# Performance work log

Measured on AMD Instinct MI355X. Metric: run time of the kernel, lower is better.

The kernel has to match this reference:

```python
import jax, jax.numpy as jnp
import numpy as np

SCALE, R_MAX, ALPHA = 16, 8, 2.0
HL, WL, C_FEAT = 16, 16, 384
HH, WH = HL * SCALE, WL * SCALE


def bilinear_resize(img, out_h, out_w):
    """PyTorch F.interpolate(mode='bilinear', align_corners=False, antialias=False).
    img: [..., H, W] -> [..., out_h, out_w]."""
    H, W = img.shape[-2], img.shape[-1]
    ys = jnp.maximum((jnp.arange(out_h, dtype=jnp.float32) + 0.5) * (H / out_h) - 0.5, 0.0)
    xs = jnp.maximum((jnp.arange(out_w, dtype=jnp.float32) + 0.5) * (W / out_w) - 0.5, 0.0)
    y0 = jnp.floor(ys).astype(jnp.int32)
    x0 = jnp.floor(xs).astype(jnp.int32)
    y1 = jnp.minimum(y0 + 1, H - 1)
    x1 = jnp.minimum(x0 + 1, W - 1)
    wy = (ys - y0)[:, None]
    wx = (xs - x0)[None, :]
    g = lambda yi, xi: img[..., yi[:, None], xi[None, :]]
    return ((1 - wy) * (1 - wx) * g(y0, x0) + (1 - wy) * wx * g(y0, x1)
            + wy * (1 - wx) * g(y1, x0) + wy * wx * g(y1, x1))


def jbu_forward(feat_lr, guide_hr, sx_raw, sy_raw, th_raw, sr_raw):
    C, Hl, Wl = feat_lr.shape[1], feat_lr.shape[2], feat_lr.shape[3]
    Hh, Wh = guide_hr.shape[2], guide_hr.shape[3]
    scale, R_max, alpha = SCALE, R_MAX, ALPHA
    NEG = -1e30  # finite stand-in for -inf (keeps grads NaN-free)

    # parameter transforms from the module
    sx = jnp.exp(sx_raw[0, 0])
    sy = jnp.exp(sy_raw[0, 0])
    th = jnp.pi * jnp.tanh(th_raw[0, 0])
    sr = jnp.exp(sr_raw[0, 0])

    Y, X = jnp.meshgrid(jnp.arange(Hh, dtype=jnp.float32),
                        jnp.arange(Wh, dtype=jnp.float32), indexing='ij')
    u = (Y + 0.5) / scale - 0.5
    v = (X + 0.5) / scale - 0.5
    uc = jnp.clip(jnp.round(u), 0, Hl - 1).astype(jnp.int32)
    vc = jnp.clip(jnp.round(v), 0, Wl - 1).astype(jnp.int32)

    sigma_eff_hr = bilinear_resize(jnp.maximum(sx, sy), Hh, Wh)
    R_map = jnp.clip(jnp.ceil(alpha * sigma_eff_hr), 1.0, float(R_max))  # [Hh,Wh]

    offs = jnp.arange(-R_max, R_max + 1, dtype=jnp.int32)
    dYg, dXg = jnp.meshgrid(offs, offs, indexing='ij')
    dY = dYg.reshape(-1)[:, None, None]  # [N,1,1]
    dX = dXg.reshape(-1)[:, None, None]

    Ui = jnp.clip(uc[None] + dY, 0, Hl - 1)  # [N,Hh,Wh]
    Vi = jnp.clip(vc[None] + dX, 0, Wl - 1)
    idx = Ui * Wl + Vi                       # flat LR index per (neighbor, HR pixel)
    gat = lambda mp: mp.reshape(-1)[idx]

    sxg = jnp.maximum(gat(sx), 1e-6)
    syg = jnp.maximum(gat(sy), 1e-6)
    thg = gat(th)
    srg = jnp.maximum(gat(sr), 1e-6)

    dx = X[None] - ((Vi.astype(jnp.float32) + 0.5) * scale - 0.5)
    dyv = Y[None] - ((Ui.astype(jnp.float32) + 0.5) * scale - 0.5)
    ct, st = jnp.cos(thg), jnp.sin(thg)
    a = dx * ct + dyv * st
    b = -dx * st + dyv * ct

    guide_lr = bilinear_resize(guide_hr[0], Hl, Wl)  # [3,Hl,Wl]
    g_diff2 = sum((guide_hr[0, c][None] - gat(guide_lr[c])) ** 2 for c in range(3))

    log_w = (-a * a / (2 * sxg ** 2 + 1e-8)
             - b * b / (2 * syg ** 2 + 1e-8)
             - g_diff2 / (2.0 * srg ** 2 + 1e-8))  # [N,Hh,Wh]

    mask = (dY * dY + dX * dX).astype(jnp.float32) <= R_map[None] ** 2
    log_w = jnp.where(mask, log_w, NEG)

    # numerically stable softmax over neighbors (== online-softmax result)
    m = log_w.max(axis=0)
    s = jnp.exp(log_w - m[None])  # masked entries underflow to 0
    den = s.sum(axis=0)           # [Hh,Wh]

    # num[c,h,w] = sum_n s[n,h,w] * feat[idx[n,h,w], c]
    # scatter neighbor weights by LR pixel, then one GEMM with the LR features
    N = idx.shape[0]
    idx2 = idx.reshape(N, Hh * Wh)
    cols = jnp.arange(Hh * Wh, dtype=jnp.int32)[None, :]
    acc = jnp.zeros((Hl * Wl, Hh * Wh), jnp.float32).at[idx2, cols].add(s.reshape(N, -1))
    feat_flat = feat_lr[0].reshape(C, Hl * Wl)  # [C, P]
    num = jnp.einsum('cp,pq->cq', feat_flat, acc).reshape(C, Hh, Wh)

    return (num / jnp.maximum(den, 1e-8)[None])[None]  # [1,C,Hh,Wh]


def setup_inputs() -> dict:
    key = jax.random.key(0)
    k1, k2, k3, k4, k5, k6 = jax.random.split(key, 6)
    feat_lr = jax.random.normal(k1, (1, C_FEAT, HL, WL), jnp.float32)
    guide_hr = jax.random.uniform(k2, (1, 3, HH, WH), dtype=jnp.float32)
    log_sigma = float(np.log(16.0))
    log_sigma_r = float(np.log(0.12))
    sx_raw = log_sigma + 0.1 * jax.random.normal(k3, (1, 1, HL, WL), jnp.float32)
    sy_raw = log_sigma + 0.1 * jax.random.normal(k4, (1, 1, HL, WL), jnp.float32)
    th_raw = 0.1 * jax.random.normal(k5, (1, 1, HL, WL), jnp.float32)
    sr_raw = log_sigma_r + 0.1 * jax.random.normal(k6, (1, 1, HL, WL), jnp.float32)
    return {"feat_lr": feat_lr, "guide_hr": guide_hr, "sx_raw": sx_raw,
            "sy_raw": sy_raw, "th_raw": th_raw, "sr_raw": sr_raw}


def reference(feat_lr, guide_hr, sx_raw, sy_raw, th_raw, sr_raw):
    return jbu_forward(feat_lr, guide_hr, sx_raw, sy_raw, th_raw, sr_raw)
```

## Files before the change

kernel.cpp:

```cpp
#include <hip/hip_runtime.h>
#include <math.h>

#define NEG_BIG  (-1e30f)
#define NEG_H16  (-60000.0f)

typedef _Float16 half8  __attribute__((ext_vector_type(8)));
typedef _Float16 half2v __attribute__((ext_vector_type(2)));
typedef float    floatx4 __attribute__((ext_vector_type(4)));

__global__ __launch_bounds__(256) void setup_all(
    const float* __restrict__ feat, const float* __restrict__ guide,
    const float* __restrict__ sx_raw, const float* __restrict__ sy_raw,
    const float* __restrict__ th_raw, const float* __restrict__ sr_raw,
    _Float16* __restrict__ feat16, float4* __restrict__ PA,
    float4* __restrict__ PB, float* __restrict__ PS,
    _Float16* __restrict__ LCtab)
{
    const int b = blockIdx.x, t = threadIdx.x;
    if (b < 384) {
        int i = b*256 + t;
        feat16[i] = (_Float16)feat[i];
        return;
    }
    if (b == 384) {
        float sx = expf(sx_raw[t]);
        float sy = expf(sy_raw[t]);
        float th = 3.14159265358979323846f * tanhf(th_raw[t]);
        float sr = expf(sr_raw[t]);
        float sxg = fmaxf(sx, 1e-6f), syg = fmaxf(sy, 1e-6f), srg = fmaxf(sr, 1e-6f);
        float iA = 1.f / (2.f*sxg*sxg + 1e-8f);
        float iB = 1.f / (2.f*syg*syg + 1e-8f);
        float iC = 1.f / (2.f*srg*srg + 1e-8f);
        float ct = cosf(th), st = sinf(th);
        float A2 = iA*ct*ct + iB*st*st;
        float B2 = 2.f*ct*st*(iA - iB);
        float C2 = iA*st*st + iB*ct*ct;
        PA[t] = make_float4(-A2, -B2, -C2, -iC);
        int i = t >> 4, j = t & 15;
        int y0 = 16*i + 7, x0 = 16*j + 7;
        float g[3];
#pragma unroll
        for (int c = 0; c < 3; ++c) {
            const float* gp = guide + c*65536;
            g[c] = 0.25f*(gp[y0*256 + x0]     + gp[y0*256 + x0 + 1] +
                          gp[(y0+1)*256 + x0] + gp[(y0+1)*256 + x0 + 1]);
        }
        PB[t] = make_float4(2.f*iC*g[0], 2.f*iC*g[1], 2.f*iC*g[2],
                            -iC*(g[0]*g[0] + g[1]*g[1] + g[2]*g[2]));
        PS[t] = fmaxf(sx, sy);
        return;
    }
    const int tb  = b - 385;
    const int uc  = tb >> 3;
    const int vc0 = (tb & 7) << 1;
    const int Pu  = t >> 4;
    const int col = t & 15;
    const int Rt  = (col >> 1) + 1;
    const int vc  = vc0 + (col & 1);
    const int R2  = Rt * Rt;
    int ylo = (Pu == 0)  ? -8 : (Pu - uc);
    int yhi = (Pu == 15) ?  8 : (Pu - uc);
    ylo = max(ylo, -8); yhi = min(yhi, 8);
    int cnt[16];
#pragma unroll
    for (int Pv = 1; Pv < 15; ++Pv) {
        int d = Pv - vc;
        int lim = R2 - d*d;
        int c = 0;
        if (lim >= 0 && ylo <= yhi) {
            int s = (int)sqrtf((float)lim);
            c = max(0, min(yhi, s) - max(ylo, -s) + 1);
        }
        cnt[Pv] = c;
    }
    cnt[0] = 0;
    if (-vc >= -8) {
        for (int dY = ylo; dY <= yhi; ++dY) {
            int lim = R2 - dY*dY;
            if (lim >= 0) {
                int r = (int)sqrtf((float)lim);
                cnt[0] += max(0, min(-vc, r) + r + 1);
            }
        }
    }
    cnt[15] = 0;
    if (15 - vc <= 8) {
        for (int dY = ylo; dY <= yhi; ++dY) {
            int lim = R2 - dY*dY;
            if (lim >= 0) {
                int r = (int)sqrtf((float)lim);
                cnt[15] += max(0, r - max(15 - vc, -r) + 1);
            }
        }
    }
    _Float16* dst = LCtab + (size_t)tb * 4096;
#pragma unroll
    for (int Pv = 0; Pv < 16; ++Pv)
        dst[(Pu*16 + Pv)*16 + col] = (_Float16)
            ((cnt[Pv] > 0) ? __logf((float)cnt[Pv]) : NEG_H16);
}

__global__ __launch_bounds__(256, 4) void jbu_main(
    const float* __restrict__ guide, const _Float16* __restrict__ feat16,
    const float4* __restrict__ PA, const float4* __restrict__ PB,
    const float* __restrict__ PS, const _Float16* __restrict__ LCtab,
    float* __restrict__ out)
{
    __shared__ float4 sPA[256];
    __shared__ float4 sPB[256];
    __shared__ __align__(16) _Float16 LCh[4096];
    __shared__ __align__(16) _Float16 Wb[32][256];
    __shared__ float redM[4][32];
    __shared__ float redD[4][32];

    const int t = threadIdx.x;
    const int q    = t & 31;
    const int grp  = t >> 5;
    const int wv   = t >> 6;
    const int Y    = blockIdx.y;
    const int X0   = blockIdx.x << 5;
    const int X    = X0 + q;
    const float Yf = (float)Y, Xf = (float)X;
    const int uc   = Y >> 4;

    sPA[t] = PA[t];
    sPB[t] = PB[t];
    {
        const float4* Lsrc =
            (const float4*)(LCtab + (size_t)(uc*8 + blockIdx.x) * 4096);
        ((float4*)LCh)[t]       = Lsrc[t];
        ((float4*)LCh)[t + 256] = Lsrc[t + 256];
    }

    float u = (Yf + 0.5f)*0.0625f - 0.5f;
    float v = (Xf + 0.5f)*0.0625f - 0.5f;
    float ysc = fmaxf(u, 0.f), xsc = fmaxf(v, 0.f);
    int y0 = (int)ysc, x0 = (int)xsc;
    int y1 = min(y0 + 1, 15), x1 = min(x0 + 1, 15);
    float wy = ysc - (float)y0, wx = xsc - (float)x0;
    float s00 = PS[y0*16 + x0], s01 = PS[y0*16 + x1];
    float s10 = PS[y1*16 + x0], s11 = PS[y1*16 + x1];
    float sig = (1.f - wy)*((1.f - wx)*s00 + wx*s01)
              +        wy *((1.f - wx)*s10 + wx*s11);
    float Rf = fminf(fmaxf(ceilf(2.f*sig), 1.f), 8.f);
    const int colq = ((int)Rf - 1)*2 + (q >> 4);

    const float g0 = guide[          (Y << 8) + X];
    const float g1 = guide[ 65536 + ((Y << 8) + X)];
    const float g2 = guide[131072 + ((Y << 8) + X)];
    const float g2s = g0*g0 + g1*g1 + g2*g2;

    __syncthreads();

    const int pbase = grp << 5;
    const float dy0  = Yf - (32.f*(float)grp + 7.5f);
    const float dy1  = dy0 - 16.f;
    const float dy20 = dy0*dy0, dy21 = dy1*dy1;
    float lw[32];
    float mloc = NEG_BIG;
#pragma unroll
    for (int col = 0; col < 16; ++col) {
        float dx    = Xf - (16.f*(float)col + 7.5f);
        float dx2   = dx*dx;
        float dxdy0 = dx*dy0, dxdy1 = dx*dy1;
#pragma unroll
        for (int row = 0; row < 2; ++row) {
            int pi = row*16 + col;
            int p  = pbase + pi;
            float4 A = sPA[p];
            float4 B = sPB[p];
            float w = fmaf(B.x, g0, B.w);
            w = fmaf(B.y, g1, w);
            w = fmaf(B.z, g2, w);
            w = fmaf(A.w, g2s, w);
            w = fmaf(A.x, dx2, w);
            w = fmaf(A.y, row ? dxdy1 : dxdy0, w);
            w = fmaf(A.z, row ? dy21  : dy20,  w);
            w += (float)LCh[p*16 + colq];
            lw[pi] = w;
            mloc = fmaxf(mloc, w);
        }
    }
    mloc = fmaxf(mloc, __shfl_xor(mloc, 32, 64));
    redM[wv][q] = mloc;
    __syncthreads();
    float m = fmaxf(fmaxf(redM[0][q], redM[1][q]),
                    fmaxf(redM[2][q], redM[3][q]));

    float dloc = 0.f;
#pragma unroll
    for (int pi = 0; pi < 32; pi += 2) {
        int p = pbase + pi;
        float e0 = __expf(lw[pi]     - m);
        float e1 = __expf(lw[pi + 1] - m);
        half2v hh; hh[0] = (_Float16)e0; hh[1] = (_Float16)e1;
        int chunk = ((p >> 3) ^ q) & 31;
        *(half2v*)&Wb[q][chunk*8 + (p & 7)] = hh;
        dloc += (float)hh[0] + (float)hh[1];
    }
    dloc += __shfl_xor(dloc, 32, 64);
    redD[wv][q] = dloc;
    __syncthreads();

    const int lane = t & 63;
    const int mrow = lane & 15;
    const int quad = lane >> 4;
    const int c0   = wv * 96;

    float idv[2];
#pragma unroll
    for (int nt = 0; nt < 2; ++nt) {
        int pix = nt*16 + mrow;
        float den = redD[0][pix] + redD[1][pix] + redD[2][pix] + redD[3][pix];
        idv[nt] = 1.f / fmaxf(den, 1e-8f);
    }

    floatx4 acc[6][2] = {};
    const _Float16* fbase = feat16 + (c0 + mrow)*256 + quad*8;

#pragma unroll
    for (int ks = 0; ks < 8; ++ks) {
        half8 a[6];
#pragma unroll
        for (int mt = 0; mt < 6; ++mt)
            a[mt] = *(const half8*)(fbase + mt*16*256 + ks*32);
        half8 b[2];
#pragma unroll
        for (int nt = 0; nt < 2; ++nt) {
            int pix = nt*16 + mrow;
            int chunk = ((ks*4 + quad) ^ pix) & 31;
            b[nt] = *(const half8*)(&Wb[pix][chunk*8]);
        }
#pragma unroll
        for (int mt = 0; mt < 6; ++mt)
#pragma unroll
            for (int nt = 0; nt < 2; ++nt)
                acc[mt][nt] = __builtin_amdgcn_mfma_f32_16x16x32_f16(
                    a[mt], b[nt], acc[mt][nt], 0, 0, 0);
    }

    float* Sf = (float*)LCh + (wv << 9);
    const int sch = lane >> 3;
    const int spg = lane & 7;
    const int outcol = (Y << 8) + X0;
#pragma unroll
    for (int mt = 0; mt < 6; ++mt) {
#pragma unroll
        for (int nt = 0; nt < 2; ++nt)
#pragma unroll
            for (int r = 0; r < 4; ++r)
                Sf[(quad*4 + r)*32 + nt*16 + mrow] = acc[mt][nt][r] * idv[nt];
#pragma unroll
        for (int j = 0; j < 2; ++j) {
            float4 vv = *(const float4*)&Sf[(j*8 + sch)*32 + spg*4];
            *(float4*)(out + (size_t)(c0 + mt*16 + j*8 + sch)*65536
                           + outcol + spg*4) = vv;
        }
    }
}

extern "C" void kernel_launch(void* const* d_in, const int* in_sizes, int n_in,
                              void* d_out, int out_size, void* d_ws, size_t ws_size,
                              hipStream_t stream)
{
    const float* feat   = (const float*)d_in[0];
    const float* guide  = (const float*)d_in[1];
    const float* sx_raw = (const float*)d_in[2];
    const float* sy_raw = (const float*)d_in[3];
    const float* th_raw = (const float*)d_in[4];
    const float* sr_raw = (const float*)d_in[5];
    float* out = (float*)d_out;

    char* ws = (char*)d_ws;
    _Float16* feat16 = (_Float16*)ws;
    float4*   PA     = (float4*)(ws + 196608);
    float4*   PB     = (float4*)(ws + 200704);
    float*    PS     = (float*)(ws + 204800);
    _Float16* LCtab  = (_Float16*)(ws + 205824);

    setup_all<<<513, 256, 0, stream>>>(feat, guide, sx_raw, sy_raw, th_raw,
                                       sr_raw, feat16, PA, PB, PS, LCtab);
    jbu_main<<<dim3(8, 256), 256, 0, stream>>>(guide, feat16, PA, PB, PS,
                                               LCtab, out);
}
```

Baseline: 158.6 us.

## Use 512-thread blocks in main kernel and vectorize feat fp16 conversion

The main kernel now runs 512 threads per block. Each thread scores 16 LR positions instead of 32, and each wave computes 48 output channels instead of 96, which halves the per-thread register arrays. The output staging buffer moves to the Wb region behind an extra barrier, and the reductions widen to 8 waves. The setup kernel converts the features to fp16 with 8-wide vector loads and stores, using far fewer blocks. The trade-off is a larger block with more barrier cost in exchange for lower register pressure per thread.

```diff
diff --git a/kernel.cpp b/kernel.cpp
--- a/kernel.cpp
+++ b/kernel.cpp
@@ -17,12 +17,17 @@
     _Float16* __restrict__ LCtab)
 {
     const int b = blockIdx.x, t = threadIdx.x;
-    if (b < 384) {
-        int i = b*256 + t;
-        feat16[i] = (_Float16)feat[i];
+    if (b < 48) {
+        int i = (b*256 + t)*8;
+        float4 f0 = *(const float4*)(feat + i);
+        float4 f1 = *(const float4*)(feat + i + 4);
+        half8 h;
+        h[0]=(_Float16)f0.x; h[1]=(_Float16)f0.y; h[2]=(_Float16)f0.z; h[3]=(_Float16)f0.w;
+        h[4]=(_Float16)f1.x; h[5]=(_Float16)f1.y; h[6]=(_Float16)f1.z; h[7]=(_Float16)f1.w;
+        *(half8*)(feat16 + i) = h;
         return;
     }
-    if (b == 384) {
+    if (b == 48) {
         float sx = expf(sx_raw[t]);
         float sy = expf(sy_raw[t]);
         float th = 3.14159265358979323846f * tanhf(th_raw[t]);
@@ -50,7 +55,7 @@
         PS[t] = fmaxf(sx, sy);
         return;
     }
-    const int tb  = b - 385;
+    const int tb  = b - 49;
     const int uc  = tb >> 3;
     const int vc0 = (tb & 7) << 1;
     const int Pu  = t >> 4;
@@ -100,36 +105,35 @@
             ((cnt[Pv] > 0) ? __logf((float)cnt[Pv]) : NEG_H16);
 }
 
-__global__ __launch_bounds__(256, 4) void jbu_main(
+__global__ __launch_bounds__(512) void jbu_main(
     const float* __restrict__ guide, const _Float16* __restrict__ feat16,
     const float4* __restrict__ PA, const float4* __restrict__ PB,
     const float* __restrict__ PS, const _Float16* __restrict__ LCtab,
     float* __restrict__ out)
 {
+    __shared__ __align__(16) _Float16 Wb[32][256];
     __shared__ float4 sPA[256];
     __shared__ float4 sPB[256];
     __shared__ __align__(16) _Float16 LCh[4096];
-    __shared__ __align__(16) _Float16 Wb[32][256];
-    __shared__ float redM[4][32];
-    __shared__ float redD[4][32];
-
-    const int t = threadIdx.x;
-    const int q    = t & 31;
-    const int grp  = t >> 5;
-    const int wv   = t >> 6;
-    const int Y    = blockIdx.y;
-    const int X0   = blockIdx.x << 5;
-    const int X    = X0 + q;
+    __shared__ float redM[8][32];
+    __shared__ float redD[8][32];
+
+    const int t   = threadIdx.x;
+    const int q   = t & 31;
+    const int grp = t >> 5;
+    const int wv  = t >> 6;
+    const int Y   = blockIdx.y;
+    const int X0  = blockIdx.x << 5;
+    const int X   = X0 + q;
     const float Yf = (float)Y, Xf = (float)X;
     const int uc   = Y >> 4;
 
-    sPA[t] = PA[t];
-    sPB[t] = PB[t];
+    if (t < 256) sPA[t] = PA[t];
+    else         sPB[t & 255] = PB[t & 255];
     {
         const float4* Lsrc =
             (const float4*)(LCtab + (size_t)(uc*8 + blockIdx.x) * 4096);
-        ((float4*)LCh)[t]       = Lsrc[t];
-        ((float4*)LCh)[t + 256] = Lsrc[t + 256];
+        ((float4*)LCh)[t] = Lsrc[t];
     }
 
     float u = (Yf + 0.5f)*0.0625f - 0.5f;
@@ -152,50 +156,45 @@
 
     __syncthreads();
 
-    const int pbase = grp << 5;
-    const float dy0  = Yf - (32.f*(float)grp + 7.5f);
-    const float dy1  = dy0 - 16.f;
-    const float dy20 = dy0*dy0, dy21 = dy1*dy1;
-    float lw[32];
+    const int pbase = grp << 4;
+    const float dy  = Yf - (16.f*(float)grp + 7.5f);
+    const float dy2 = dy*dy;
+    float lw[16];
     float mloc = NEG_BIG;
 #pragma unroll
     for (int col = 0; col < 16; ++col) {
-        float dx    = Xf - (16.f*(float)col + 7.5f);
-        float dx2   = dx*dx;
-        float dxdy0 = dx*dy0, dxdy1 = dx*dy1;
-#pragma unroll
-        for (int row = 0; row < 2; ++row) {
-            int pi = row*16 + col;
-            int p  = pbase + pi;
-            float4 A = sPA[p];
-            float4 B = sPB[p];
-            float w = fmaf(B.x, g0, B.w);
-            w = fmaf(B.y, g1, w);
-            w = fmaf(B.z, g2, w);
-            w = fmaf(A.w, g2s, w);
-            w = fmaf(A.x, dx2, w);
-            w = fmaf(A.y, row ? dxdy1 : dxdy0, w);
-            w = fmaf(A.z, row ? dy21  : dy20,  w);
-            w += (float)LCh[p*16 + colq];
-            lw[pi] = w;
-            mloc = fmaxf(mloc, w);
-        }
+        int p = pbase + col;
+        float dx = Xf - (16.f*(float)col + 7.5f);
+        float4 A = sPA[p];
+        float4 B = sPB[p];
+        float w = fmaf(B.x, g0, B.w);
+        w = fmaf(B.y, g1, w);
+        w = fmaf(B.z, g2, w);
+        w = fmaf(A.w, g2s, w);
+        w = fmaf(A.x, dx*dx, w);
+        w = fmaf(A.y, dx*dy, w);
+        w = fmaf(A.z, dy2, w);
+        w += (float)LCh[p*16 + colq];
+        lw[col] = w;
+        mloc = fmaxf(mloc, w);
     }
     mloc = fmaxf(mloc, __shfl_xor(mloc, 32, 64));
     redM[wv][q] = mloc;
     __syncthreads();
-    float m = fmaxf(fmaxf(redM[0][q], redM[1][q]),
-                    fmaxf(redM[2][q], redM[3][q]));
+    const float m = fmaxf(fmaxf(fmaxf(redM[0][q], redM[1][q]),
+                                fmaxf(redM[2][q], redM[3][q])),
+                          fmaxf(fmaxf(redM[4][q], redM[5][q]),
+                                fmaxf(redM[6][q], redM[7][q])));
 
     float dloc = 0.f;
 #pragma unroll
-    for (int pi = 0; pi < 32; pi += 2) {
-        int p = pbase + pi;
-        float e0 = __expf(lw[pi]     - m);
-        float e1 = __expf(lw[pi + 1] - m);
+    for (int col = 0; col < 16; col += 2) {
+        int p0 = pbase + col;
+        float e0 = __expf(lw[col]     - m);
+        float e1 = __expf(lw[col + 1] - m);
         half2v hh; hh[0] = (_Float16)e0; hh[1] = (_Float16)e1;
-        int chunk = ((p >> 3) ^ q) & 31;
-        *(half2v*)&Wb[q][chunk*8 + (p & 7)] = hh;
+        int chunk = ((p0 >> 3) ^ q) & 31;
+        *(half2v*)&Wb[q][chunk*8 + (p0 & 7)] = hh;
         dloc += (float)hh[0] + (float)hh[1];
     }
     dloc += __shfl_xor(dloc, 32, 64);
@@ -205,24 +204,25 @@
     const int lane = t & 63;
     const int mrow = lane & 15;
     const int quad = lane >> 4;
-    const int c0   = wv * 96;
+    const int c0   = wv * 48;
 
     float idv[2];
 #pragma unroll
     for (int nt = 0; nt < 2; ++nt) {
         int pix = nt*16 + mrow;
-        float den = redD[0][pix] + redD[1][pix] + redD[2][pix] + redD[3][pix];
+        float den = ((redD[0][pix] + redD[1][pix]) + (redD[2][pix] + redD[3][pix]))
+                  + ((redD[4][pix] + redD[5][pix]) + (redD[6][pix] + redD[7][pix]));
         idv[nt] = 1.f / fmaxf(den, 1e-8f);
     }
 
-    floatx4 acc[6][2] = {};
+    floatx4 acc[3][2] = {};
     const _Float16* fbase = feat16 + (c0 + mrow)*256 + quad*8;
 
 #pragma unroll
     for (int ks = 0; ks < 8; ++ks) {
-        half8 a[6];
-#pragma unroll
-        for (int mt = 0; mt < 6; ++mt)
+        half8 a[3];
+#pragma unroll
+        for (int mt = 0; mt < 3; ++mt)
             a[mt] = *(const half8*)(fbase + mt*16*256 + ks*32);
         half8 b[2];
 #pragma unroll
@@ -232,19 +232,21 @@
             b[nt] = *(const half8*)(&Wb[pix][chunk*8]);
         }
 #pragma unroll
-        for (int mt = 0; mt < 6; ++mt)
+        for (int mt = 0; mt < 3; ++mt)
 #pragma unroll
             for (int nt = 0; nt < 2; ++nt)
                 acc[mt][nt] = __builtin_amdgcn_mfma_f32_16x16x32_f16(
                     a[mt], b[nt], acc[mt][nt], 0, 0, 0);
     }
 
-    float* Sf = (float*)LCh + (wv << 9);
+    __syncthreads();
+
+    float* Sf = (float*)Wb + (wv << 9);
     const int sch = lane >> 3;
     const int spg = lane & 7;
     const int outcol = (Y << 8) + X0;
 #pragma unroll
-    for (int mt = 0; mt < 6; ++mt) {
+    for (int mt = 0; mt < 3; ++mt) {
 #pragma unroll
         for (int nt = 0; nt < 2; ++nt)
 #pragma unroll
@@ -278,8 +280,8 @@
     float*    PS     = (float*)(ws + 204800);
     _Float16* LCtab  = (_Float16*)(ws + 205824);
 
-    setup_all<<<513, 256, 0, stream>>>(feat, guide, sx_raw, sy_raw, th_raw,
+    setup_all<<<177, 256, 0, stream>>>(feat, guide, sx_raw, sy_raw, th_raw,
                                        sr_raw, feat16, PA, PB, PS, LCtab);
-    jbu_main<<<dim3(8, 256), 256, 0, stream>>>(guide, feat16, PA, PB, PS,
+    jbu_main<<<dim3(8, 256), 512, 0, stream>>>(guide, feat16, PA, PB, PS,
                                                LCtab, out);
 }
```

New measurement: 161.8 us. +2.0%, slower.
